# Optimization experiments

Measured on AMD Instinct MI355X. Metric: run time of the kernel, lower is better.

Reference implementation:

```python
import jax, jax.numpy as jnp
import numpy as np

B, L, H = 8, 64, 128


def setup_inputs() -> dict:
    key = jax.random.key(0)
    ks = jax.random.split(key, 9)
    s = 1.0 / np.sqrt(H)

    def lin(k, shape):
        return jax.random.uniform(k, shape, jnp.float32, -s, s)

    return {
        "words_feats": jax.random.normal(ks[0], (B, L, H), jnp.float32),
        "words_masks": jnp.ones((B, L), jnp.int32),
        "Wl": lin(ks[1], (H, 1)), "bl": lin(ks[2], (1,)),
        "Wr": lin(ks[3], (H, 1)), "br": lin(ks[4], (1,)),
        "Wrep": lin(ks[5], (H, H)), "brep": lin(ks[6], (H,)),
        "Ws": lin(ks[7], (H, 1)), "bs": lin(ks[8], (1,)),
    }


def reference(words_feats, words_masks, Wl, bl, Wr, br, Wrep, brep, Ws, bs):
    # CYK chart DP. All sentences have full length L (masks all ones), so the
    # chart recursion runs L-1 levels with static trip count.
    Bsz, Ln, Hd = words_feats.shape
    ks_ = jnp.arange(Ln)  # split point k
    js_ = jnp.arange(Ln)  # start position j

    # chart T[b, i, j] = feature of span starting at j with length i+1
    T0 = jnp.zeros((Bsz, Ln, Ln, Hd), words_feats.dtype).at[:, 0].set(words_feats)

    def body(T, i):
        # left child:  T[b, k, j]            -> [B, k, j, H]
        left = T
        # right child: T[b, i-k-1, j+k+1]    -> [B, k, j, H] (clipped; masked below)
        rows = jnp.clip(i - ks_ - 1, 0, Ln - 1)                       # [k]
        cols = jnp.clip(js_[None, :] + ks_[:, None] + 1, 0, Ln - 1)   # [k, j]
        right = T[:, rows[:, None], cols]                             # [B, k, j, H]

        # 2-way attention combine of (left, right)
        sl = left @ Wl + bl                                            # [B, k, j, 1]
        sr = right @ Wr + br
        w = jax.nn.softmax(jnp.concatenate([sl, sr], axis=-1), axis=-1)
        h_hat = w[..., :1] * left + w[..., 1:] * right                 # [B, k, j, H]
        temp = jax.nn.relu(h_hat @ Wrep + brep) + h_hat

        # only k < i splits and spans with i + j < L exist; others are exact
        # zeros (matching the torch zero-initialized temp_h table)
        valid = (ks_[:, None] < i) & (js_[None, :] + i < Ln)           # [k, j]
        temp = jnp.where(valid[None, :, :, None], temp, 0.0)

        # softmax over ALL L split rows (zero rows contribute bias logits,
        # exactly as in the torch code)
        logits = (temp @ Ws + bs)[..., 0]                              # [B, k, j]
        split = jax.nn.softmax(logits, axis=1)                         # over k
        new_row = jnp.einsum('bkj,bkjh->bjh', split, temp)             # [B, j, H]
        new_row = jnp.where((js_ + i < Ln)[None, :, None], new_row, 0.0)
        return T.at[:, i].set(new_row), None

    T, _ = jax.lax.scan(body, T0, jnp.arange(1, Ln))
    return T[:, Ln - 1, 0]  # sentence feature: full span starting at 0
```

## Files before the change

kernel.cpp:

```cpp
#include <hip/hip_runtime.h>
#include <math.h>

#define Hd 128
#define Ln 64
#define Bsz 8
#define NTHR 512
#define NBLK (8 * 63)


typedef __attribute__((ext_vector_type(8))) short short8v;
typedef __attribute__((ext_vector_type(4))) float f32x4;

__global__ void init_kernel(const float* __restrict__ wf, float* __restrict__ T,
                            int* __restrict__ flg) {
    int idx = blockIdx.x * 256 + threadIdx.x;
    int b = idx >> 13;
    int rest = idx & 8191;
    T[(size_t)b * (Ln * Ln * Hd) + rest] = wf[idx];
    if (idx < Bsz * Ln * Ln) flg[idx] = 0;
}

__device__ __forceinline__ float2 ld_row8(const float* p) {
    unsigned long long v = __hip_atomic_load((const unsigned long long*)p,
                                             __ATOMIC_RELAXED, __HIP_MEMORY_SCOPE_AGENT);
    return __builtin_bit_cast(float2, v);
}

__device__ __forceinline__ void wait_flag(const int* p) {
    while (__hip_atomic_load(p, __ATOMIC_RELAXED, __HIP_MEMORY_SCOPE_AGENT) == 0)
        __builtin_amdgcn_s_sleep(1);
    asm volatile("" ::: "memory");
}

__device__ __forceinline__ void bf_split3(float x, unsigned short& a0,
                                          unsigned short& a1, unsigned short& a2) {
    unsigned u0 = __builtin_bit_cast(unsigned, x);
    a0 = (unsigned short)(u0 >> 16);
    float f0 = __builtin_bit_cast(float, u0 & 0xffff0000u);
    float r1 = x - f0;
    unsigned u1 = __builtin_bit_cast(unsigned, r1);
    a1 = (unsigned short)(u1 >> 16);
    float f1 = __builtin_bit_cast(float, u1 & 0xffff0000u);
    float r2 = r1 - f1;
    a2 = (unsigned short)(__builtin_bit_cast(unsigned, r2) >> 16);
}

__device__ __forceinline__ float bfval(unsigned short v) {
    return __builtin_bit_cast(float, ((unsigned)v) << 16);
}

#define KSTEP(SK, B0_, B1_, B2_)                                                \
    {                                                                           \
        int off = ((16 * ch + (ln & 15)) << 7) +                                \
                  ((((SK << 2) + (ln >> 4)) ^ (ln & 15)) << 3);                 \
        short8v a0 = *(const short8v*)&sH0[off];                                \
        short8v a1 = *(const short8v*)&sH1[off];                                \
        short8v a2 = *(const short8v*)&sH2[off];                                \
        acc = __builtin_amdgcn_mfma_f32_16x16x32_bf16(a0, B0_, acc, 0, 0, 0);   \
        acc = __builtin_amdgcn_mfma_f32_16x16x32_bf16(a0, B1_, acc, 0, 0, 0);   \
        acc = __builtin_amdgcn_mfma_f32_16x16x32_bf16(a1, B0_, acc, 0, 0, 0);   \
        acc = __builtin_amdgcn_mfma_f32_16x16x32_bf16(a0, B2_, acc, 0, 0, 0);   \
        acc = __builtin_amdgcn_mfma_f32_16x16x32_bf16(a1, B1_, acc, 0, 0, 0);   \
        acc = __builtin_amdgcn_mfma_f32_16x16x32_bf16(a2, B0_, acc, 0, 0, 0);   \
    }

template<int NCH>
__device__ __forceinline__ void do_cell(
    int i, int jj, int b, int wv, int ln, int tid,
    const float* __restrict__ Tb, float* __restrict__ T, float* __restrict__ out,
    int* __restrict__ flgb,
    unsigned short* __restrict__ sH0, unsigned short* __restrict__ sH1,
    unsigned short* __restrict__ sH2,
    float* __restrict__ sR, float (*part)[Ln],
    const short8v (&B0)[4], const short8v (&B1)[4], const short8v (&B2)[4],
    float2 wlv, float2 wrv, float bl, float br, float bs, float wsc, float bbc)
{
    constexpr int NR = 2 * NCH;

    if (i >= 2) wait_flag(&flgb[(i - 1) * Ln + jj]);

    float2 Lr[NR], Rr[NR];
    #pragma unroll
    for (int r = 0; r < NR; ++r) {
        int k = wv + 8 * r;
        int kcl = k < i ? k : i - 1;
        Lr[r] = ld_row8(Tb + ((size_t)kcl * Ln + jj) * Hd + 2 * ln);
        Rr[r] = *(const float2*)&sR[((i - 1 - kcl) << 7) + 2 * ln];
    }
    float pl[NR], pr[NR];
    #pragma unroll
    for (int r = 0; r < NR; ++r) {
        pl[r] = Lr[r].x * wlv.x + Lr[r].y * wlv.y;
        pr[r] = Rr[r].x * wrv.x + Rr[r].y * wrv.y;
    }
    #pragma unroll
    for (int off2 = 32; off2 > 0; off2 >>= 1) {
        #pragma unroll
        for (int r = 0; r < NR; ++r) {
            pl[r] += __shfl_xor(pl[r], off2);
            pr[r] += __shfl_xor(pr[r], off2);
        }
    }
    #pragma unroll
    for (int r = 0; r < NR; ++r) {
        int k = wv + 8 * r;
        float sl = pl[r] + bl, sr2 = pr[r] + br;
        float mm = fmaxf(sl, sr2);
        float e0 = __expf(sl - mm), e1 = __expf(sr2 - mm);
        float inv = 1.f / (e0 + e1);
        float w0 = e0 * inv, w1 = e1 * inv;
        float h0 = w0 * Lr[r].x + w1 * Rr[r].x;
        float h1 = w0 * Lr[r].y + w1 * Rr[r].y;
        unsigned short x0, x1, x2, y0, y1, y2;
        bf_split3(h0, x0, x1, x2);
        bf_split3(h1, y0, y1, y2);
        int off = (k << 7) + ((((ln >> 2)) ^ (k & 15)) << 3) + ((2 * ln) & 7);
        *(unsigned*)&sH0[off] = (unsigned)x0 | ((unsigned)y0 << 16);
        *(unsigned*)&sH1[off] = (unsigned)x1 | ((unsigned)y1 << 16);
        *(unsigned*)&sH2[off] = (unsigned)x2 | ((unsigned)y2 << 16);
    }
    __syncthreads();

    const int colc = 16 * wv + (ln & 15);
    float tmp[NCH][4];
    #pragma unroll
    for (int ch = 0; ch < NCH; ++ch) {
        f32x4 acc = {0.f, 0.f, 0.f, 0.f};
        KSTEP(0, B0[0], B1[0], B2[0])
        KSTEP(1, B0[1], B1[1], B2[1])
        KSTEP(2, B0[2], B1[2], B2[2])
        KSTEP(3, B0[3], B1[3], B2[3])
        float p[4];
        #pragma unroll
        for (int q = 0; q < 4; ++q) {
            int krow = 16 * ch + (ln >> 4) * 4 + q;
            int offh = (krow << 7) + (((colc >> 3) ^ (krow & 15)) << 3) + (colc & 7);
            float h = (bfval(sH0[offh]) + bfval(sH1[offh])) + bfval(sH2[offh]);
            float t = fmaxf(acc[q] + bbc, 0.f) + h;
            tmp[ch][q] = t;
            p[q] = t * wsc;
        }
        #pragma unroll
        for (int off2 = 1; off2 <= 8; off2 <<= 1) {
            #pragma unroll
            for (int q = 0; q < 4; ++q) p[q] += __shfl_xor(p[q], off2);
        }
        if ((ln & 15) == 0) {
            #pragma unroll
            for (int q = 0; q < 4; ++q)
                part[wv][16 * ch + (ln >> 4) * 4 + q] = p[q];
        }
    }
    __syncthreads();

    float lgv = -INFINITY;
    if (ln < i) {
        float ss = ((part[0][ln] + part[1][ln]) + (part[2][ln] + part[3][ln]))
                 + ((part[4][ln] + part[5][ln]) + (part[6][ln] + part[7][ln]));
        lgv = ss + bs;
    }
    float M = lgv;
    #pragma unroll
    for (int off2 = 32; off2 > 0; off2 >>= 1) M = fmaxf(M, __shfl_xor(M, off2));
    M = fmaxf(M, bs);
    float e = (ln < i) ? __expf(lgv - M) : 0.f;
    float S = e;
    #pragma unroll
    for (int off2 = 32; off2 > 0; off2 >>= 1) S += __shfl_xor(S, off2);
    float den = S + (float)(Ln - i) * __expf(bs - M);

    float v = 0.f;
    #pragma unroll
    for (int ch = 0; ch < NCH; ++ch) {
        #pragma unroll
        for (int q = 0; q < 4; ++q) {
            int krow = 16 * ch + (ln >> 4) * 4 + q;
            v += __shfl(e, krow) * tmp[ch][q];
        }
    }
    v += __shfl_xor(v, 16);
    v += __shfl_xor(v, 32);
    if (ln < 16) {
        float res = v / den;
        __hip_atomic_store(&T[(((size_t)b * Ln + i) * Ln + jj) * Hd + colc], res,
                           __ATOMIC_RELAXED, __HIP_MEMORY_SCOPE_AGENT);
        sR[(i << 7) + colc] = res;
        if (i == Ln - 1) out[b * Hd + colc] = res;
    }
    __syncthreads();
    if (tid == 0)
        __hip_atomic_store(&flgb[i * Ln + jj], 1, __ATOMIC_RELAXED,
                           __HIP_MEMORY_SCOPE_AGENT);
}

__global__ __launch_bounds__(NTHR, 2)
void glt_df(const float* __restrict__ Wl, const float* __restrict__ blp,
            const float* __restrict__ Wr, const float* __restrict__ brp,
            const float* __restrict__ Wrep, const float* __restrict__ brepp,
            const float* __restrict__ Wsv, const float* __restrict__ bsp,
            float* __restrict__ T, int* __restrict__ flg, float* __restrict__ out)
{
    __shared__ __align__(16) unsigned short sH0[Ln * Hd];
    __shared__ __align__(16) unsigned short sH1[Ln * Hd];
    __shared__ __align__(16) unsigned short sH2[Ln * Hd];
    __shared__ __align__(16) float sR[Ln * Hd];
    __shared__ float part[8][Ln];

    const int tid = threadIdx.x;
    const int wv  = tid >> 6;
    const int ln  = tid & 63;
    const int b   = blockIdx.x & 7;
    const int D   = (blockIdx.x >> 3) + 1;

    const int bcol = 16 * wv + (ln & 15);
    short8v B0[4], B1[4], B2[4];
    #pragma unroll
    for (int sk = 0; sk < 4; ++sk) {
        #pragma unroll
        for (int jx = 0; jx < 8; ++jx) {
            int k = 32 * sk + (ln >> 4) * 8 + jx;
            float w = Wrep[k * Hd + bcol];
            unsigned short w0, w1, w2;
            bf_split3(w, w0, w1, w2);
            B0[sk][jx] = (short)w0;
            B1[sk][jx] = (short)w1;
            B2[sk][jx] = (short)w2;
        }
    }

    const float bl = blp[0], br = brp[0], bs = bsp[0];
    const float2 wlv = *(const float2*)&Wl[2 * ln];
    const float2 wrv = *(const float2*)&Wr[2 * ln];
    const float wsc = Wsv[bcol];
    const float bbc = brepp[bcol];

    const float* Tb = T + (size_t)b * (Ln * Ln * Hd);
    int* flgb = flg + b * (Ln * Ln);

    if (wv == 0)
        *(float2*)&sR[2 * ln] = ld_row8(Tb + (size_t)D * Hd + 2 * ln);
    __syncthreads();

    for (int i = 1; i <= D; ++i) {
        const int jj = D - i;
        switch ((i + 15) >> 4) {
            case 1: do_cell<1>(i, jj, b, wv, ln, tid, Tb, T, out, flgb,
                               sH0, sH1, sH2, sR, part, B0, B1, B2,
                               wlv, wrv, bl, br, bs, wsc, bbc); break;
            case 2: do_cell<2>(i, jj, b, wv, ln, tid, Tb, T, out, flgb,
                               sH0, sH1, sH2, sR, part, B0, B1, B2,
                               wlv, wrv, bl, br, bs, wsc, bbc); break;
            case 3: do_cell<3>(i, jj, b, wv, ln, tid, Tb, T, out, flgb,
                               sH0, sH1, sH2, sR, part, B0, B1, B2,
                               wlv, wrv, bl, br, bs, wsc, bbc); break;
            default: do_cell<4>(i, jj, b, wv, ln, tid, Tb, T, out, flgb,
                                sH0, sH1, sH2, sR, part, B0, B1, B2,
                                wlv, wrv, bl, br, bs, wsc, bbc); break;
        }
    }
}

extern "C" void kernel_launch(void* const* d_in, const int* in_sizes, int n_in,
                              void* d_out, int out_size, void* d_ws, size_t ws_size,
                              hipStream_t stream)
{
    const float* wf   = (const float*)d_in[0];
    const float* Wl   = (const float*)d_in[2];
    const float* bl   = (const float*)d_in[3];
    const float* Wr   = (const float*)d_in[4];
    const float* br   = (const float*)d_in[5];
    const float* Wrep = (const float*)d_in[6];
    const float* brep = (const float*)d_in[7];
    const float* Ws   = (const float*)d_in[8];
    const float* bs   = (const float*)d_in[9];

    float* T   = (float*)d_ws;
    int*   flg = (int*)((char*)d_ws + (size_t)Bsz * Ln * Ln * Hd * 4);
    float* out = (float*)d_out;

    init_kernel<<<256, 256, 0, stream>>>(wf, T, flg);
    glt_df<<<NBLK, NTHR, 0, stream>>>(Wl, bl, Wr, br, Wrep, brep, Ws, bs,
                                      T, flg, out);
}
```

Before: 509.4 us.

## Assign each block a fixed span start and cache left children in LDS

Each block now walks one chart column: fixed start jj, span lengths rising from 1. Before, each block walked an anti-diagonal with a fixed span end. The block's own earlier results are the left children, and the first 48 rows of them are kept in a smaller LDS buffer. Right children are now read from global memory with atomic loads, and each cell waits on the flag of the neighbouring column's previous cell. The smaller LDS footprint may ease occupancy, in exchange for more global traffic on right-child reads and a different cross-block dependency pattern.

Result: no change. 510.1 us (+0.1%).

```diff
diff --git a/kernel.cpp b/kernel.cpp
--- a/kernel.cpp
+++ b/kernel.cpp
@@ -5,7 +5,7 @@
 #define Ln 64
 #define Bsz 8
 #define NTHR 512
-#define NBLK (8 * 63)
+#define NBLK 512
 
 
 typedef __attribute__((ext_vector_type(8))) short short8v;
@@ -71,21 +71,22 @@
     int* __restrict__ flgb,
     unsigned short* __restrict__ sH0, unsigned short* __restrict__ sH1,
     unsigned short* __restrict__ sH2,
-    float* __restrict__ sR, float (*part)[Ln],
+    float* __restrict__ sL, float (*part)[Ln],
     const short8v (&B0)[4], const short8v (&B1)[4], const short8v (&B2)[4],
     float2 wlv, float2 wrv, float bl, float br, float bs, float wsc, float bbc)
 {
     constexpr int NR = 2 * NCH;
 
-    if (i >= 2) wait_flag(&flgb[(i - 1) * Ln + jj]);
+    if (i >= 2) wait_flag(&flgb[(i - 1) * Ln + jj + 1]);
 
     float2 Lr[NR], Rr[NR];
     #pragma unroll
     for (int r = 0; r < NR; ++r) {
         int k = wv + 8 * r;
         int kcl = k < i ? k : i - 1;
-        Lr[r] = ld_row8(Tb + ((size_t)kcl * Ln + jj) * Hd + 2 * ln);
-        Rr[r] = *(const float2*)&sR[((i - 1 - kcl) << 7) + 2 * ln];
+        Lr[r] = (kcl < 48) ? *(const float2*)&sL[(kcl << 7) + 2 * ln]
+                           : ld_row8(Tb + ((size_t)kcl * Ln + jj) * Hd + 2 * ln);
+        Rr[r] = ld_row8(Tb + ((size_t)(i - 1 - kcl) * Ln + (jj + kcl + 1)) * Hd + 2 * ln);
     }
     float pl[NR], pr[NR];
     #pragma unroll
@@ -114,7 +115,7 @@
         unsigned short x0, x1, x2, y0, y1, y2;
         bf_split3(h0, x0, x1, x2);
         bf_split3(h1, y0, y1, y2);
-        int off = (k << 7) + ((((ln >> 2)) ^ (k & 15)) << 3) + ((2 * ln) & 7);
+        int off = (k << 7) + (((ln >> 2) ^ (k & 15)) << 3) + ((2 * ln) & 7);
         *(unsigned*)&sH0[off] = (unsigned)x0 | ((unsigned)y0 << 16);
         *(unsigned*)&sH1[off] = (unsigned)x1 | ((unsigned)y1 << 16);
         *(unsigned*)&sH2[off] = (unsigned)x2 | ((unsigned)y2 << 16);
@@ -184,7 +185,7 @@
         float res = v / den;
         __hip_atomic_store(&T[(((size_t)b * Ln + i) * Ln + jj) * Hd + colc], res,
                            __ATOMIC_RELAXED, __HIP_MEMORY_SCOPE_AGENT);
-        sR[(i << 7) + colc] = res;
+        if (i < 48) sL[(i << 7) + colc] = res;
         if (i == Ln - 1) out[b * Hd + colc] = res;
     }
     __syncthreads();
@@ -203,14 +204,17 @@
     __shared__ __align__(16) unsigned short sH0[Ln * Hd];
     __shared__ __align__(16) unsigned short sH1[Ln * Hd];
     __shared__ __align__(16) unsigned short sH2[Ln * Hd];
-    __shared__ __align__(16) float sR[Ln * Hd];
+    __shared__ __align__(16) float sL[48 * Hd];
     __shared__ float part[8][Ln];
 
     const int tid = threadIdx.x;
     const int wv  = tid >> 6;
     const int ln  = tid & 63;
     const int b   = blockIdx.x & 7;
-    const int D   = (blockIdx.x >> 3) + 1;
+    const int p   = blockIdx.x >> 3;
+    const int jj  = 63 - p;
+
+    if (p == 0) return;
 
     const int bcol = 16 * wv + (ln & 15);
     short8v B0[4], B1[4], B2[4];
@@ -238,23 +242,22 @@
     int* flgb = flg + b * (Ln * Ln);
 
     if (wv == 0)
-        *(float2*)&sR[2 * ln] = ld_row8(Tb + (size_t)D * Hd + 2 * ln);
-    __syncthreads();
-
-    for (int i = 1; i <= D; ++i) {
-        const int jj = D - i;
+        *(float2*)&sL[2 * ln] = ld_row8(Tb + (size_t)jj * Hd + 2 * ln);
+    __syncthreads();
+
+    for (int i = 1; i <= p; ++i) {
         switch ((i + 15) >> 4) {
             case 1: do_cell<1>(i, jj, b, wv, ln, tid, Tb, T, out, flgb,
-                               sH0, sH1, sH2, sR, part, B0, B1, B2,
+                               sH0, sH1, sH2, sL, part, B0, B1, B2,
                                wlv, wrv, bl, br, bs, wsc, bbc); break;
             case 2: do_cell<2>(i, jj, b, wv, ln, tid, Tb, T, out, flgb,
-                               sH0, sH1, sH2, sR, part, B0, B1, B2,
+                               sH0, sH1, sH2, sL, part, B0, B1, B2,
                                wlv, wrv, bl, br, bs, wsc, bbc); break;
             case 3: do_cell<3>(i, jj, b, wv, ln, tid, Tb, T, out, flgb,
-                               sH0, sH1, sH2, sR, part, B0, B1, B2,
+                               sH0, sH1, sH2, sL, part, B0, B1, B2,
                                wlv, wrv, bl, br, bs, wsc, bbc); break;
             default: do_cell<4>(i, jj, b, wv, ln, tid, Tb, T, out, flgb,
-                                sH0, sH1, sH2, sR, part, B0, B1, B2,
+                                sH0, sH1, sH2, sL, part, B0, B1, B2,
                                 wlv, wrv, bl, br, bs, wsc, bbc); break;
         }
     }
```
